# Optimization experiments

Measured on AMD Instinct MI355X. Metric: run time of the kernel, lower is better.

## Reference

```python
import jax, jax.numpy as jnp
import numpy as np

TEMPERATURE = 0.04
EPS = 1e-6

def _conv_valid(x, k, groups=1):
    # x: [N,C,H,W], k: [O,I,kh,kw]
    return jax.lax.conv_general_dilated(
        x, k, window_strides=(1, 1), padding='VALID',
        dimension_numbers=('NCHW', 'OIHW', 'NCHW'),
        feature_group_count=groups)

def setup_inputs() -> dict:
    key = jax.random.key(0)
    k1, k2 = jax.random.split(key)
    roi_piece = jax.random.normal(k1, (256, 1, 17, 17), dtype=jnp.float32)
    roi_background = jax.random.normal(k2, (256, 1, 384, 384), dtype=jnp.float32)
    return {"roi_piece": roi_piece, "roi_background": roi_background}

def reference(roi_piece, roi_background):
    B, _, Ht, Wt = roi_piece.shape
    Hi, Wi = roi_background.shape[-2:]
    Lh, Lw = Hi - Ht + 1, Wi - Wt + 1
    n = Ht * Wt

    # --- template normalization (torch .std is unbiased, ddof=1) ---
    t = roi_piece - jnp.mean(roi_piece, axis=(2, 3), keepdims=True)
    t_std = jnp.maximum(jnp.sqrt(jnp.var(t, axis=(2, 3), keepdims=True, ddof=1)), EPS)
    t_norm = t / t_std  # [B,1,Ht,Wt], zero-mean per batch

    # --- fast ZNCC: since sum(t_norm)==0, corr = corr(image, t_norm) / window_std ---
    # per-batch cross-correlation via grouped conv: batch -> channels/groups
    num = _conv_valid(roi_background.reshape(1, B, Hi, Wi), t_norm, groups=B)[0]  # [B,Lh,Lw]

    # sliding-window mean/var via box filters (var unbiased=False, clamped then sqrt)
    ones_k = jnp.ones((1, 1, Ht, Wt), dtype=roi_background.dtype)
    s1 = _conv_valid(roi_background, ones_k)        # [B,1,Lh,Lw]
    s2 = _conv_valid(roi_background * roi_background, ones_k)
    mu = s1 / n
    var = jnp.maximum(s2 / n - mu * mu, EPS)
    std = jnp.sqrt(var)[:, 0]                        # [B,Lh,Lw]

    corr = num / std  # [B,Lh,Lw]

    # --- soft-argmax over the correlation map ---
    probs = jax.nn.softmax(corr.reshape(B, -1) / TEMPERATURE, axis=-1).reshape(B, Lh, Lw)
    y_coords = jnp.arange(Lh, dtype=corr.dtype)
    x_coords = jnp.arange(Lw, dtype=corr.dtype)
    expected_y = jnp.einsum('bhw,h->b', probs, y_coords)
    expected_x = jnp.einsum('bhw,w->b', probs, x_coords)
    offset_y = expected_y - (Lh - 1) / 2.0
    offset_x = expected_x - (Lw - 1) / 2.0
    offset = jnp.stack([offset_x, offset_y], axis=1)  # [B,2]

    max_corr = jnp.max(corr, axis=(1, 2))             # [B]
    return offset, max_corr
```

## Files before the change

### kernel.cpp

```cpp
#include <hip/hip_runtime.h>
#include <math.h>

#define NB 256
#define HT 17
#define WT 17
#define HI 384
#define WI 384
#define LH 368
#define LW 368
#define NTEMPL 289
#define TPAD 20
#define TY 32
#define TX 128
#define NTXT 3
#define NTYT 12
#define NTILES 36
#define BR 48
#define BP 144
#define TEMP_INV 25.0f
#define EPSV 1e-6f

__global__ __launch_bounds__(256) void tmpl_norm_kernel(
    const float* __restrict__ piece, float* __restrict__ tn) {
    int b = blockIdx.x;
    const float* x = piece + b * NTEMPL;
    int tid = threadIdx.x;
    int wid = tid >> 6, lane = tid & 63;

    float v0 = (tid < NTEMPL) ? x[tid] : 0.f;
    float v1 = (tid + 256 < NTEMPL) ? x[tid + 256] : 0.f;

    __shared__ float sred[4];
    float s = v0 + v1;
    #pragma unroll
    for (int o = 32; o > 0; o >>= 1) s += __shfl_down(s, o, 64);
    if (lane == 0) sred[wid] = s;
    __syncthreads();
    float mean = (sred[0] + sred[1] + sred[2] + sred[3]) * (1.0f / NTEMPL);

    float d0 = (tid < NTEMPL) ? (v0 - mean) : 0.f;
    float d1 = (tid + 256 < NTEMPL) ? (v1 - mean) : 0.f;
    float q = d0 * d0 + d1 * d1;
    __syncthreads();
    #pragma unroll
    for (int o = 32; o > 0; o >>= 1) q += __shfl_down(q, o, 64);
    if (lane == 0) sred[wid] = q;
    __syncthreads();
    float var = (sred[0] + sred[1] + sred[2] + sred[3]) * (1.0f / (NTEMPL - 1));
    float stdv = sqrtf(var);
    if (stdv < EPSV) stdv = EPSV;
    float inv = 1.0f / stdv;

    float* o = tn + b * (HT * TPAD);
    for (int sIdx = tid; sIdx < HT * TPAD; sIdx += 256) {
        int i = sIdx / TPAD, j = sIdx % TPAD;
        o[sIdx] = (j < WT) ? (x[i * WT + j] - mean) * inv : 0.f;
    }
}

template<int P, bool LAST>
__device__ __forceinline__ void corr_step(
    int i, int tr, int xb,
    const float* __restrict__ tp,
    const float (*__restrict__ bg)[BP],
    float (&w)[4][TPAD], float (&ttf)[2][TPAD], float (&acc)[4][4])
{
    if (!LAST) {
        const float4* tq = (const float4*)(tp + (i + 1) * TPAD);
        #pragma unroll
        for (int q = 0; q < 5; ++q) ((float4*)ttf[(P & 1) ^ 1])[q] = tq[q];
    }
    const float* tc = ttf[P & 1];
    #pragma unroll
    for (int j = 0; j < 17; ++j) {
        float tv = tc[j];
        #pragma unroll
        for (int k = 0; k < 4; ++k) acc[0][k] = fmaf(tv, w[P][j + k], acc[0][k]);
    }
    if (!LAST) {
        const float4* br = (const float4*)&bg[tr + i + 4][xb];
        #pragma unroll
        for (int q = 0; q < 5; ++q) ((float4*)w[P])[q] = br[q];
    }
    #pragma unroll
    for (int e = 1; e < 4; ++e) {
        #pragma unroll
        for (int j = 0; j < 17; ++j) {
            float tv = tc[j];
            #pragma unroll
            for (int k = 0; k < 4; ++k)
                acc[e][k] = fmaf(tv, w[(P + e) & 3][j + k], acc[e][k]);
        }
    }
}

__global__ __launch_bounds__(256, 2) void corr_kernel(
    const float* __restrict__ bgg, const float* __restrict__ tn,
    float* __restrict__ partials) {
    int blk = blockIdx.x;
    int b = blk / NTILES;
    int t = blk % NTILES;
    int ty0 = (t / NTXT) * TY;
    int tx0 = (t % NTXT) * TX;
    const float* img = bgg + (size_t)b * HI * WI;
    const float* tp  = tn + b * (HT * TPAD);

    __shared__ float bg[BR][BP];
    __shared__ float c1[TY][BP];
    __shared__ float c2[TY][BP];
    __shared__ float redm[4], redl[4], redy[4], redx[4];

    int tid = threadIdx.x;
    int wid = tid >> 6, lane = tid & 63;

    for (int l = tid; l < BR * (BP / 4); l += 256) {
        int r = l / (BP / 4), c = (l % (BP / 4)) * 4;
        int iy = ty0 + r, ix = tx0 + c;
        float4 v = make_float4(0.f, 0.f, 0.f, 0.f);
        if (iy < HI && ix < WI) v = *(const float4*)(img + iy * WI + ix);
        *(float4*)&bg[r][c] = v;
    }
    __syncthreads();

    for (int task = tid; task < 2 * BP; task += 256) {
        int half = (task >= BP) ? 1 : 0;
        int cc = task - half * BP;
        int r0 = half * 16;
        float s = 0.f, s2 = 0.f;
        #pragma unroll
        for (int i2 = 0; i2 < HT; ++i2) { float v = bg[r0 + i2][cc]; s += v; s2 = fmaf(v, v, s2); }
        c1[r0][cc] = s; c2[r0][cc] = s2;
        for (int r = r0 + 1; r < r0 + 16; ++r) {
            float vn = bg[r + 16][cc], vo = bg[r - 1][cc];
            s += vn - vo; s2 += vn * vn - vo * vo;
            c1[r][cc] = s; c2[r][cc] = s2;
        }
    }
    __syncthreads();

    int tr = (tid >> 5) * 4;
    int xb = (tid & 31) * 4;
    float w[4][TPAD];
    float ttf[2][TPAD];
    float acc[4][4] = {};

    #pragma unroll
    for (int m = 0; m < 4; ++m) {
        const float4* br = (const float4*)&bg[tr + m][xb];
        #pragma unroll
        for (int q = 0; q < 5; ++q) ((float4*)w[m])[q] = br[q];
    }
    {
        const float4* t0 = (const float4*)tp;
        #pragma unroll
        for (int q = 0; q < 5; ++q) ((float4*)ttf[0])[q] = t0[q];
    }

    for (int i = 0; i < 16; i += 4) {
        corr_step<0, false>(i,     tr, xb, tp, bg, w, ttf, acc);
        corr_step<1, false>(i + 1, tr, xb, tp, bg, w, ttf, acc);
        corr_step<2, false>(i + 2, tr, xb, tp, bg, w, ttf, acc);
        corr_step<3, false>(i + 3, tr, xb, tp, bg, w, ttf, acc);
    }
    corr_step<0, true>(16, tr, xb, tp, bg, w, ttf, acc);

    const float invn = 1.0f / NTEMPL;
    float corr[4][4];
    float m = -INFINITY;
    #pragma unroll
    for (int e = 0; e < 4; ++e) {
        float cc1f[TPAD], cc2f[TPAD];
        const float4* a1 = (const float4*)&c1[tr + e][xb];
        const float4* a2 = (const float4*)&c2[tr + e][xb];
        #pragma unroll
        for (int q = 0; q < 5; ++q) { ((float4*)cc1f)[q] = a1[q]; ((float4*)cc2f)[q] = a2[q]; }
        float s1 = 0.f, s2 = 0.f;
        #pragma unroll
        for (int j = 0; j < HT; ++j) { s1 += cc1f[j]; s2 += cc2f[j]; }
        int oy = ty0 + tr + e;
        #pragma unroll
        for (int k = 0; k < 4; ++k) {
            float mu = s1 * invn;
            float var = s2 * invn - mu * mu;
            if (var < EPSV) var = EPSV;
            float cv = acc[e][k] / sqrtf(var);
            int ox = tx0 + xb + k;
            if (oy < LH && ox < LW) m = fmaxf(m, cv);
            else cv = -INFINITY;
            corr[e][k] = cv;
            if (k < 3) {
                s1 += cc1f[k + HT] - cc1f[k];
                s2 += cc2f[k + HT] - cc2f[k];
            }
        }
    }

    float mm = m;
    #pragma unroll
    for (int o = 32; o > 0; o >>= 1) mm = fmaxf(mm, __shfl_down(mm, o, 64));
    if (lane == 0) redm[wid] = mm;
    __syncthreads();
    float M = fmaxf(fmaxf(redm[0], redm[1]), fmaxf(redm[2], redm[3]));

    float l = 0.f, sy = 0.f, sx = 0.f;
    #pragma unroll
    for (int e = 0; e < 4; ++e) {
        int oy = ty0 + tr + e;
        #pragma unroll
        for (int k = 0; k < 4; ++k) {
            float cv = corr[e][k];
            float ev = (cv == -INFINITY) ? 0.f : __expf((cv - M) * TEMP_INV);
            l += ev;
            sy = fmaf(ev, (float)oy, sy);
            sx = fmaf(ev, (float)(tx0 + xb + k), sx);
        }
    }
    #pragma unroll
    for (int o = 32; o > 0; o >>= 1) {
        l  += __shfl_down(l, o, 64);
        sy += __shfl_down(sy, o, 64);
        sx += __shfl_down(sx, o, 64);
    }
    if (lane == 0) { redl[wid] = l; redy[wid] = sy; redx[wid] = sx; }
    __syncthreads();
    if (tid == 0) {
        float* p = partials + (size_t)blk * 4;
        p[0] = M;
        p[1] = redl[0] + redl[1] + redl[2] + redl[3];
        p[2] = redy[0] + redy[1] + redy[2] + redy[3];
        p[3] = redx[0] + redx[1] + redx[2] + redx[3];
    }
}

__global__ __launch_bounds__(256) void reduce_kernel(
    const float* __restrict__ partials, float* __restrict__ out) {
    int b = blockIdx.x;
    int tid = threadIdx.x;
    int wid = tid >> 6, lane = tid & 63;

    float m = -INFINITY, l = 0.f, sy = 0.f, sx = 0.f;
    if (tid < NTILES) {
        const float* p = partials + (size_t)(b * NTILES + tid) * 4;
        m = p[0]; l = p[1]; sy = p[2]; sx = p[3];
    }
    __shared__ float rm[4], rl[4], ry[4], rx[4];
    float mm = m;
    #pragma unroll
    for (int o = 32; o > 0; o >>= 1) mm = fmaxf(mm, __shfl_down(mm, o, 64));
    if (lane == 0) rm[wid] = mm;
    __syncthreads();
    float M = fmaxf(fmaxf(rm[0], rm[1]), fmaxf(rm[2], rm[3]));

    float sc = (m == -INFINITY) ? 0.f : __expf((m - M) * TEMP_INV);
    l *= sc; sy *= sc; sx *= sc;
    #pragma unroll
    for (int o = 32; o > 0; o >>= 1) {
        l  += __shfl_down(l, o, 64);
        sy += __shfl_down(sy, o, 64);
        sx += __shfl_down(sx, o, 64);
    }
    if (lane == 0) { rl[wid] = l; ry[wid] = sy; rx[wid] = sx; }
    __syncthreads();
    if (tid == 0) {
        float L  = rl[0] + rl[1] + rl[2] + rl[3];
        float SY = ry[0] + ry[1] + ry[2] + ry[3];
        float SX = rx[0] + rx[1] + rx[2] + rx[3];
        out[b * 2 + 0] = SX / L - 183.5f;
        out[b * 2 + 1] = SY / L - 183.5f;
        out[2 * NB + b] = M;
    }
}

extern "C" void kernel_launch(void* const* d_in, const int* in_sizes, int n_in,
                              void* d_out, int out_size, void* d_ws, size_t ws_size,
                              hipStream_t stream) {
    const float* piece = (const float*)d_in[0];
    const float* bgg   = (const float*)d_in[1];
    float* out = (float*)d_out;

    float* tn = (float*)d_ws;
    float* partials = tn + NB * HT * TPAD;

    tmpl_norm_kernel<<<NB, 256, 0, stream>>>(piece, tn);
    corr_kernel<<<NB * NTILES, 256, 0, stream>>>(bgg, tn, partials);
    reduce_kernel<<<NB, 256, 0, stream>>>(partials, out);
}
```

Before: 519.7 us.

## Shrink box-filter LDS buffer to one reused half-tile to raise occupancy

```diff
diff --git a/kernel.cpp b/kernel.cpp
--- a/kernel.cpp
+++ b/kernel.cpp
@@ -94,7 +94,47 @@
     }
 }
 
-__global__ __launch_bounds__(256, 2) void corr_kernel(
+template<bool SQ>
+__device__ __forceinline__ void build_half(
+    const float (*__restrict__ bg)[BP], float (*__restrict__ cb)[BP],
+    int r0, int cc)
+{
+    float s = 0.f;
+    #pragma unroll
+    for (int i2 = 0; i2 < HT; ++i2) {
+        float v = bg[r0 + i2][cc];
+        if (SQ) s = fmaf(v, v, s); else s += v;
+    }
+    cb[0][cc] = s;
+    for (int r = 1; r < 16; ++r) {
+        float vn = bg[r0 + r + 16][cc], vo = bg[r0 + r - 1][cc];
+        if (SQ) s += vn * vn - vo * vo; else s += vn - vo;
+        cb[r][cc] = s;
+    }
+}
+
+__device__ __forceinline__ void consume_half(
+    const float (*__restrict__ cb)[BP], int row0, int xb, float (&sv)[4][4])
+{
+    #pragma unroll
+    for (int e = 0; e < 4; ++e) {
+        float cf[TPAD];
+        const float4* a = (const float4*)&cb[row0 + e][xb];
+        #pragma unroll
+        for (int q = 0; q < 5; ++q) ((float4*)cf)[q] = a[q];
+        float s = 0.f;
+        #pragma unroll
+        for (int j = 0; j < HT; ++j) s += cf[j];
+        sv[e][0] = s;
+        #pragma unroll
+        for (int k = 1; k < 4; ++k) {
+            s += cf[k - 1 + HT] - cf[k - 1];
+            sv[e][k] = s;
+        }
+    }
+}
+
+__global__ __launch_bounds__(256, 4) void corr_kernel(
     const float* __restrict__ bgg, const float* __restrict__ tn,
     float* __restrict__ partials) {
     int blk = blockIdx.x;
@@ -106,8 +146,7 @@
     const float* tp  = tn + b * (HT * TPAD);
 
     __shared__ float bg[BR][BP];
-    __shared__ float c1[TY][BP];
-    __shared__ float c2[TY][BP];
+    __shared__ float cb[16][BP];
     __shared__ float redm[4], redl[4], redy[4], redx[4];
 
     int tid = threadIdx.x;
@@ -122,22 +161,6 @@
     }
     __syncthreads();
 
-    for (int task = tid; task < 2 * BP; task += 256) {
-        int half = (task >= BP) ? 1 : 0;
-        int cc = task - half * BP;
-        int r0 = half * 16;
-        float s = 0.f, s2 = 0.f;
-        #pragma unroll
-        for (int i2 = 0; i2 < HT; ++i2) { float v = bg[r0 + i2][cc]; s += v; s2 = fmaf(v, v, s2); }
-        c1[r0][cc] = s; c2[r0][cc] = s2;
-        for (int r = r0 + 1; r < r0 + 16; ++r) {
-            float vn = bg[r + 16][cc], vo = bg[r - 1][cc];
-            s += vn - vo; s2 += vn * vn - vo * vo;
-            c1[r][cc] = s; c2[r][cc] = s2;
-        }
-    }
-    __syncthreads();
-
     int tr = (tid >> 5) * 4;
     int xb = (tid & 31) * 4;
     float w[4][TPAD];
@@ -164,34 +187,42 @@
     }
     corr_step<0, true>(16, tr, xb, tp, bg, w, ttf, acc);
 
+    bool lowHalf = (tr < 16);
+    int  row0    = lowHalf ? tr : (tr - 16);
+    float s1v[4][4], s2v[4][4];
+
+    if (tid < BP) build_half<false>(bg, cb, 0, tid);
+    __syncthreads();
+    if (lowHalf) consume_half(cb, row0, xb, s1v);
+    __syncthreads();
+    if (tid < BP) build_half<false>(bg, cb, 16, tid);
+    __syncthreads();
+    if (!lowHalf) consume_half(cb, row0, xb, s1v);
+    __syncthreads();
+    if (tid < BP) build_half<true>(bg, cb, 0, tid);
+    __syncthreads();
+    if (lowHalf) consume_half(cb, row0, xb, s2v);
+    __syncthreads();
+    if (tid < BP) build_half<true>(bg, cb, 16, tid);
+    __syncthreads();
+    if (!lowHalf) consume_half(cb, row0, xb, s2v);
+
     const float invn = 1.0f / NTEMPL;
     float corr[4][4];
     float m = -INFINITY;
     #pragma unroll
     for (int e = 0; e < 4; ++e) {
-        float cc1f[TPAD], cc2f[TPAD];
-        const float4* a1 = (const float4*)&c1[tr + e][xb];
-        const float4* a2 = (const float4*)&c2[tr + e][xb];
-        #pragma unroll
-        for (int q = 0; q < 5; ++q) { ((float4*)cc1f)[q] = a1[q]; ((float4*)cc2f)[q] = a2[q]; }
-        float s1 = 0.f, s2 = 0.f;
-        #pragma unroll
-        for (int j = 0; j < HT; ++j) { s1 += cc1f[j]; s2 += cc2f[j]; }
         int oy = ty0 + tr + e;
         #pragma unroll
         for (int k = 0; k < 4; ++k) {
-            float mu = s1 * invn;
-            float var = s2 * invn - mu * mu;
+            float mu = s1v[e][k] * invn;
+            float var = s2v[e][k] * invn - mu * mu;
             if (var < EPSV) var = EPSV;
             float cv = acc[e][k] / sqrtf(var);
             int ox = tx0 + xb + k;
             if (oy < LH && ox < LW) m = fmaxf(m, cv);
             else cv = -INFINITY;
             corr[e][k] = cv;
-            if (k < 3) {
-                s1 += cc1f[k + HT] - cc1f[k];
-                s2 += cc2f[k + HT] - cc2f[k];
-            }
         }
     }
 
```

New measurement: 734.0 us. 41.2% more time.

## Compute correlation with split-bf16 MFMA Toeplitz GEMM on 64x64 tiles

Applied to the files above, without the earlier changes.

```diff
diff --git a/kernel.cpp b/kernel.cpp
--- a/kernel.cpp
+++ b/kernel.cpp
@@ -10,15 +10,28 @@
 #define LW 368
 #define NTEMPL 289
 #define TPAD 20
-#define TY 32
-#define TX 128
-#define NTXT 3
-#define NTYT 12
+#define BM 64
+#define BN 64
+#define NXB 6
 #define NTILES 36
-#define BR 48
-#define BP 144
+#define BGR 80
+#define BGC 80
+#define PHB 88
+#define RP 65
 #define TEMP_INV 25.0f
 #define EPSV 1e-6f
+
+typedef __attribute__((ext_vector_type(8))) short bf16x8;
+typedef __attribute__((ext_vector_type(4))) float f32x4;
+
+__device__ __forceinline__ unsigned short f2bf(float x) {
+    unsigned u = __float_as_uint(x);
+    u += 0x7FFF + ((u >> 16) & 1);
+    return (unsigned short)(u >> 16);
+}
+__device__ __forceinline__ float bf2f(unsigned short h) {
+    return __uint_as_float(((unsigned)h) << 16);
+}
 
 __global__ __launch_bounds__(256) void tmpl_norm_kernel(
     const float* __restrict__ piece, float* __restrict__ tn) {
@@ -58,41 +71,18 @@
     }
 }
 
-template<int P, bool LAST>
-__device__ __forceinline__ void corr_step(
-    int i, int tr, int xb,
-    const float* __restrict__ tp,
-    const float (*__restrict__ bg)[BP],
-    float (&w)[4][TPAD], float (&ttf)[2][TPAD], float (&acc)[4][4])
-{
-    if (!LAST) {
-        const float4* tq = (const float4*)(tp + (i + 1) * TPAD);
-        #pragma unroll
-        for (int q = 0; q < 5; ++q) ((float4*)ttf[(P & 1) ^ 1])[q] = tq[q];
-    }
-    const float* tc = ttf[P & 1];
-    #pragma unroll
-    for (int j = 0; j < 17; ++j) {
-        float tv = tc[j];
-        #pragma unroll
-        for (int k = 0; k < 4; ++k) acc[0][k] = fmaf(tv, w[P][j + k], acc[0][k]);
-    }
-    if (!LAST) {
-        const float4* br = (const float4*)&bg[tr + i + 4][xb];
-        #pragma unroll
-        for (int q = 0; q < 5; ++q) ((float4*)w[P])[q] = br[q];
-    }
-    #pragma unroll
-    for (int e = 1; e < 4; ++e) {
-        #pragma unroll
-        for (int j = 0; j < 17; ++j) {
-            float tv = tc[j];
-            #pragma unroll
-            for (int k = 0; k < 4; ++k)
-                acc[e][k] = fmaf(tv, w[(P + e) & 3][j + k], acc[e][k]);
-        }
-    }
-}
+struct SMainT {
+    unsigned short bh[BGR][PHB];
+    unsigned short bl[BGR][PHB];
+    unsigned short Bh[17 * 512];
+    unsigned short Bl[17 * 512];
+};
+struct SStatT {
+    unsigned short pad0[BGR][PHB];
+    unsigned short pad1[BGR][PHB];
+    float r[BGR][RP];
+};
+union SU { SMainT m; SStatT s; };
 
 __global__ __launch_bounds__(256, 2) void corr_kernel(
     const float* __restrict__ bgg, const float* __restrict__ tn,
@@ -100,98 +90,162 @@
     int blk = blockIdx.x;
     int b = blk / NTILES;
     int t = blk % NTILES;
-    int ty0 = (t / NTXT) * TY;
-    int tx0 = (t % NTXT) * TX;
+    int y0 = (t / NXB) * BM;
+    int x0 = (t % NXB) * BN;
     const float* img = bgg + (size_t)b * HI * WI;
     const float* tp  = tn + b * (HT * TPAD);
 
-    __shared__ float bg[BR][BP];
-    __shared__ float c1[TY][BP];
-    __shared__ float c2[TY][BP];
+    __shared__ SU S;
     __shared__ float redm[4], redl[4], redy[4], redx[4];
 
     int tid = threadIdx.x;
     int wid = tid >> 6, lane = tid & 63;
-
-    for (int l = tid; l < BR * (BP / 4); l += 256) {
-        int r = l / (BP / 4), c = (l % (BP / 4)) * 4;
-        int iy = ty0 + r, ix = tx0 + c;
+    int lm = lane & 15, lk = lane >> 4;
+    int wy = wid >> 1, wx = wid & 1;
+    int y0w = wy * 32, x0w = wx * 32;
+
+    for (int l = tid; l < BGR * (BGC / 4); l += 256) {
+        int r = l / (BGC / 4), c4 = (l % (BGC / 4)) * 4;
+        int iy = y0 + r, ix = x0 + c4;
         float4 v = make_float4(0.f, 0.f, 0.f, 0.f);
         if (iy < HI && ix < WI) v = *(const float4*)(img + iy * WI + ix);
-        *(float4*)&bg[r][c] = v;
-    }
-    __syncthreads();
-
-    for (int task = tid; task < 2 * BP; task += 256) {
-        int half = (task >= BP) ? 1 : 0;
-        int cc = task - half * BP;
-        int r0 = half * 16;
-        float s = 0.f, s2 = 0.f;
-        #pragma unroll
-        for (int i2 = 0; i2 < HT; ++i2) { float v = bg[r0 + i2][cc]; s += v; s2 = fmaf(v, v, s2); }
-        c1[r0][cc] = s; c2[r0][cc] = s2;
-        for (int r = r0 + 1; r < r0 + 16; ++r) {
-            float vn = bg[r + 16][cc], vo = bg[r - 1][cc];
-            s += vn - vo; s2 += vn * vn - vo * vo;
-            c1[r][cc] = s; c2[r][cc] = s2;
-        }
-    }
-    __syncthreads();
-
-    int tr = (tid >> 5) * 4;
-    int xb = (tid & 31) * 4;
-    float w[4][TPAD];
-    float ttf[2][TPAD];
-    float acc[4][4] = {};
-
-    #pragma unroll
-    for (int m = 0; m < 4; ++m) {
-        const float4* br = (const float4*)&bg[tr + m][xb];
-        #pragma unroll
-        for (int q = 0; q < 5; ++q) ((float4*)w[m])[q] = br[q];
-    }
-    {
-        const float4* t0 = (const float4*)tp;
-        #pragma unroll
-        for (int q = 0; q < 5; ++q) ((float4*)ttf[0])[q] = t0[q];
-    }
-
-    for (int i = 0; i < 16; i += 4) {
-        corr_step<0, false>(i,     tr, xb, tp, bg, w, ttf, acc);
-        corr_step<1, false>(i + 1, tr, xb, tp, bg, w, ttf, acc);
-        corr_step<2, false>(i + 2, tr, xb, tp, bg, w, ttf, acc);
-        corr_step<3, false>(i + 3, tr, xb, tp, bg, w, ttf, acc);
-    }
-    corr_step<0, true>(16, tr, xb, tp, bg, w, ttf, acc);
+        unsigned short h[4], lo[4];
+        float vv[4] = {v.x, v.y, v.z, v.w};
+        #pragma unroll
+        for (int e = 0; e < 4; ++e) {
+            h[e] = f2bf(vv[e]);
+            lo[e] = f2bf(vv[e] - bf2f(h[e]));
+        }
+        *(uint2*)&S.m.bh[r][c4] = *(const uint2*)h;
+        *(uint2*)&S.m.bl[r][c4] = *(const uint2*)lo;
+    }
+
+    for (int e = tid; e < 17 * 512; e += 256) {
+        int i   = e >> 9;
+        int rem = e & 511;
+        int kc  = rem >> 7;
+        int n   = (rem >> 3) & 15;
+        int e8  = rem & 7;
+        int j   = kc * 8 + e8 - n;
+        float val = (j >= 0 && j < 17) ? tp[i * TPAD + j] : 0.f;
+        unsigned short h = f2bf(val);
+        S.m.Bh[e] = h;
+        S.m.Bl[e] = f2bf(val - bf2f(h));
+    }
+    __syncthreads();
+
+    f32x4 accM[2][2] = {};
+    f32x4 accC[2][2] = {};
+    for (int i = 0; i < HT; ++i) {
+        int bb = i * 512 + lk * 128 + lm * 8;
+        bf16x8 Bh_ = *(const bf16x8*)&S.m.Bh[bb];
+        bf16x8 Bl_ = *(const bf16x8*)&S.m.Bl[bb];
+        #pragma unroll
+        for (int mt = 0; mt < 2; ++mt) {
+            int row = y0w + mt * 16 + lm + i;
+            #pragma unroll
+            for (int nt = 0; nt < 2; ++nt) {
+                int col = x0w + nt * 16 + lk * 8;
+                bf16x8 Ah = *(const bf16x8*)&S.m.bh[row][col];
+                bf16x8 Al = *(const bf16x8*)&S.m.bl[row][col];
+                accM[mt][nt] = __builtin_amdgcn_mfma_f32_16x16x32_bf16(
+                    Ah, Bh_, accM[mt][nt], 0, 0, 0);
+                accC[mt][nt] = __builtin_amdgcn_mfma_f32_16x16x32_bf16(
+                    Ah, Bl_, accC[mt][nt], 0, 0, 0);
+                accC[mt][nt] = __builtin_amdgcn_mfma_f32_16x16x32_bf16(
+                    Al, Bh_, accC[mt][nt], 0, 0, 0);
+            }
+        }
+    }
+    __syncthreads();
+
+    for (int task = tid; task < BGR * 2; task += 256) {
+        int r = task >> 1, xh = (task & 1) * 32;
+        float s = 0.f;
+        #pragma unroll
+        for (int j = 0; j < HT; ++j)
+            s += bf2f(S.m.bh[r][xh + j]) + bf2f(S.m.bl[r][xh + j]);
+        S.s.r[r][xh] = s;
+        for (int x = xh + 1; x < xh + 32; ++x) {
+            s += bf2f(S.m.bh[r][x + 16]) + bf2f(S.m.bl[r][x + 16])
+               - bf2f(S.m.bh[r][x - 1]) - bf2f(S.m.bl[r][x - 1]);
+            S.s.r[r][x] = s;
+        }
+    }
+    __syncthreads();
+    float s1v[2][2][4];
+    #pragma unroll
+    for (int mt = 0; mt < 2; ++mt)
+    #pragma unroll
+    for (int nt = 0; nt < 2; ++nt) {
+        int xcol = x0w + nt * 16 + lm;
+        int yb = y0w + mt * 16 + lk * 4;
+        float s = 0.f;
+        #pragma unroll
+        for (int ii = 0; ii < HT; ++ii) s += S.s.r[yb + ii][xcol];
+        s1v[mt][nt][0] = s;
+        #pragma unroll
+        for (int q = 1; q < 4; ++q) {
+            s += S.s.r[yb + q + 16][xcol] - S.s.r[yb + q - 1][xcol];
+            s1v[mt][nt][q] = s;
+        }
+    }
+    __syncthreads();
+
+    for (int task = tid; task < BGR * 2; task += 256) {
+        int r = task >> 1, xh = (task & 1) * 32;
+        float s = 0.f;
+        #pragma unroll
+        for (int j = 0; j < HT; ++j) {
+            float v = bf2f(S.m.bh[r][xh + j]) + bf2f(S.m.bl[r][xh + j]);
+            s = fmaf(v, v, s);
+        }
+        S.s.r[r][xh] = s;
+        for (int x = xh + 1; x < xh + 32; ++x) {
+            float vn = bf2f(S.m.bh[r][x + 16]) + bf2f(S.m.bl[r][x + 16]);
+            float vo = bf2f(S.m.bh[r][x - 1]) + bf2f(S.m.bl[r][x - 1]);
+            s += vn * vn - vo * vo;
+            S.s.r[r][x] = s;
+        }
+    }
+    __syncthreads();
+    float s2v[2][2][4];
+    #pragma unroll
+    for (int mt = 0; mt < 2; ++mt)
+    #pragma unroll
+    for (int nt = 0; nt < 2; ++nt) {
+        int xcol = x0w + nt * 16 + lm;
+        int yb = y0w + mt * 16 + lk * 4;
+        float s = 0.f;
+        #pragma unroll
+        for (int ii = 0; ii < HT; ++ii) s += S.s.r[yb + ii][xcol];
+        s2v[mt][nt][0] = s;
+        #pragma unroll
+        for (int q = 1; q < 4; ++q) {
+            s += S.s.r[yb + q + 16][xcol] - S.s.r[yb + q - 1][xcol];
+            s2v[mt][nt][q] = s;
+        }
+    }
 
     const float invn = 1.0f / NTEMPL;
-    float corr[4][4];
+    float corr[2][2][4];
     float m = -INFINITY;
     #pragma unroll
-    for (int e = 0; e < 4; ++e) {
-        float cc1f[TPAD], cc2f[TPAD];
-        const float4* a1 = (const float4*)&c1[tr + e][xb];
-        const float4* a2 = (const float4*)&c2[tr + e][xb];
-        #pragma unroll
-        for (int q = 0; q < 5; ++q) { ((float4*)cc1f)[q] = a1[q]; ((float4*)cc2f)[q] = a2[q]; }
-        float s1 = 0.f, s2 = 0.f;
-        #pragma unroll
-        for (int j = 0; j < HT; ++j) { s1 += cc1f[j]; s2 += cc2f[j]; }
-        int oy = ty0 + tr + e;
-        #pragma unroll
-        for (int k = 0; k < 4; ++k) {
-            float mu = s1 * invn;
-            float var = s2 * invn - mu * mu;
+    for (int mt = 0; mt < 2; ++mt)
+    #pragma unroll
+    for (int nt = 0; nt < 2; ++nt) {
+        int ox = x0 + x0w + nt * 16 + lm;
+        #pragma unroll
+        for (int q = 0; q < 4; ++q) {
+            int oy = y0 + y0w + mt * 16 + lk * 4 + q;
+            float num = accM[mt][nt][q] + accC[mt][nt][q];
+            float mu = s1v[mt][nt][q] * invn;
+            float var = s2v[mt][nt][q] * invn - mu * mu;
             if (var < EPSV) var = EPSV;
-            float cv = acc[e][k] / sqrtf(var);
-            int ox = tx0 + xb + k;
+            float cv = num / sqrtf(var);
             if (oy < LH && ox < LW) m = fmaxf(m, cv);
             else cv = -INFINITY;
-            corr[e][k] = cv;
-            if (k < 3) {
-                s1 += cc1f[k + HT] - cc1f[k];
-                s2 += cc2f[k + HT] - cc2f[k];
-            }
+            corr[mt][nt][q] = cv;
         }
     }
 
@@ -204,15 +258,18 @@
 
     float l = 0.f, sy = 0.f, sx = 0.f;
     #pragma unroll
-    for (int e = 0; e < 4; ++e) {
-        int oy = ty0 + tr + e;
-        #pragma unroll
-        for (int k = 0; k < 4; ++k) {
-            float cv = corr[e][k];
+    for (int mt = 0; mt < 2; ++mt)
+    #pragma unroll
+    for (int nt = 0; nt < 2; ++nt) {
+        int ox = x0 + x0w + nt * 16 + lm;
+        #pragma unroll
+        for (int q = 0; q < 4; ++q) {
+            int oy = y0 + y0w + mt * 16 + lk * 4 + q;
+            float cv = corr[mt][nt][q];
             float ev = (cv == -INFINITY) ? 0.f : __expf((cv - M) * TEMP_INV);
             l += ev;
             sy = fmaf(ev, (float)oy, sy);
-            sx = fmaf(ev, (float)(tx0 + xb + k), sx);
+            sx = fmaf(ev, (float)ox, sx);
         }
     }
     #pragma unroll
```

Result: slower. 828.7 us (+59.4%).
